# Kernel optimization log

Hardware: AMD Instinct MI355X
Metric: run time of the kernel (lower is better)

Reference implementation:

```python
import jax, jax.numpy as jnp
import numpy as np

N_NODES = 16384
N_EDGES = 131072
N_GRAPHS = 64
DIMS = [396, 4096, 2048, 1024, 1024, 2048, 256, 1]  # layer widths from __init__
BN_EPS = 1e-5


def setup_inputs() -> dict:
    key = jax.random.key(0)
    ks = jax.random.split(key, 32)
    inp = {
        "x": jax.random.normal(ks[0], (N_NODES, DIMS[0]), jnp.float32),
        "edge_index": jax.random.randint(ks[1], (2, N_EDGES), 0, N_NODES, dtype=jnp.int32),
        "batch": jnp.sort(jax.random.randint(ks[2], (N_NODES,), 0, N_GRAPHS, dtype=jnp.int32)),
    }
    for i in range(7):
        fi, fo = DIMS[i], DIMS[i + 1]
        inp[f"W{i+1}"] = jax.random.normal(ks[3 + i], (fi, fo), jnp.float32) * (1.0 / np.sqrt(fi)).astype(np.float32)
        inp[f"b{i+1}"] = jnp.zeros((fo,), jnp.float32)
    for i in range(6):
        inp[f"g{i+1}"] = jnp.ones((DIMS[i + 1],), jnp.float32)
        inp[f"be{i+1}"] = jnp.zeros((DIMS[i + 1],), jnp.float32)
    return inp


def _gcn_norm(edge_index, n):
    # PyG GCNConv default: add self-loops, sym-normalize D^-1/2 (A+I) D^-1/2
    loop = jnp.arange(n, dtype=edge_index.dtype)
    src = jnp.concatenate([edge_index[0], loop])
    dst = jnp.concatenate([edge_index[1], loop])
    deg = jax.ops.segment_sum(jnp.ones_like(src, jnp.float32), dst, num_segments=n)
    dinv = jax.lax.rsqrt(jnp.maximum(deg, 1.0))  # deg >= 1 due to self-loops
    norm = dinv[src] * dinv[dst]  # [E + N]
    return src, dst, norm


def _gcn_conv(x, W, b, src, dst, norm, n):
    h = x @ W                                   # dense linear transform
    msg = h[src] * norm[:, None]                # gather + edge scaling
    agg = jax.ops.segment_sum(msg, dst, num_segments=n)  # scatter-add
    return agg + b


def _bn(x, g, b):
    # BatchNorm1d in training mode: biased batch variance
    m = jnp.mean(x, axis=0)
    v = jnp.mean(jnp.square(x - m), axis=0)
    return (x - m) * jax.lax.rsqrt(v + BN_EPS) * g + b


def reference(x, edge_index, batch,
              W1, b1, W2, b2, W3, b3, W4, b4, W5, b5, W6, b6, W7, b7,
              g1, be1, g2, be2, g3, be3, g4, be4, g5, be5, g6, be6):
    n = x.shape[0]
    src, dst, norm = _gcn_norm(edge_index, n)
    Ws = [W1, W2, W3, W4, W5, W6]
    bs = [b1, b2, b3, b4, b5, b6]
    gs = [g1, g2, g3, g4, g5, g6]
    bes = [be1, be2, be3, be4, be5, be6]
    h = x
    for W, b, g, be in zip(Ws, bs, gs, bes):
        h = jax.nn.relu(_gcn_conv(h, W, b, src, dst, norm, n))
        h = _bn(h, g, be)
    h = _gcn_conv(h, W7, b7, src, dst, norm, n)   # [N, 1], no relu/bn
    out = jax.ops.segment_sum(h, batch, num_segments=N_GRAPHS)  # global_add_pool
    return out
```

## Files before the change

kernel.cpp:

```cpp
#include <hip/hip_runtime.h>


#define NN 16384
#define NE 131072
#define NG 64

typedef unsigned int u32;
typedef unsigned short u16;
typedef __attribute__((ext_vector_type(8))) _Float16 half8;
typedef __attribute__((ext_vector_type(4))) float f32x4;
typedef __attribute__((ext_vector_type(8))) u16 us8;
typedef __attribute__((ext_vector_type(4))) u16 us4;
typedef __attribute__((ext_vector_type(2))) u16 us2;

#define AS1(p) ((const __attribute__((address_space(1))) void*)(p))
#define AS3(p) ((__attribute__((address_space(3))) void*)(p))

__device__ __forceinline__ float b2f(u16 h) {
    _Float16 x = __builtin_bit_cast(_Float16, h);
    return (float)x;
}
__device__ __forceinline__ u16 f2b(float f) {
    _Float16 x = (_Float16)f;
    return __builtin_bit_cast(u16, x);
}

template <int VW> struct VecU;
template <> struct VecU<8> { typedef us8 T; };
template <> struct VecU<4> { typedef us4 T; };
template <> struct VecU<2> { typedef us2 T; };
template <> struct VecU<1> { typedef u16 T; };

template <int VW>
__device__ __forceinline__ void loadf(const u16* p, float* f) {
    typename VecU<VW>::T v = *(const typename VecU<VW>::T*)p;
    if constexpr (VW == 1) {
        f[0] = b2f((u16)v);
    } else {
        #pragma unroll
        for (int j = 0; j < VW; ++j) f[j] = b2f(v[j]);
    }
}
template <int VW>
__device__ __forceinline__ void storef(u16* p, const float* f) {
    typename VecU<VW>::T v;
    if constexpr (VW == 1) {
        v = f2b(f[0]);
    } else {
        #pragma unroll
        for (int j = 0; j < VW; ++j) v[j] = f2b(f[j]);
    }
    *(typename VecU<VW>::T*)p = v;
}

__global__ void k_degi(const int* __restrict__ dst, int* __restrict__ deg) {
    int e = blockIdx.x * 256 + threadIdx.x;
    if (e < NE) atomicAdd(&deg[dst[e]], 1);
}
__global__ void k_nrm(const int* __restrict__ src, const int* __restrict__ dst,
                      const float* __restrict__ dinv, float* __restrict__ nrm) {
    int e = blockIdx.x * 256 + threadIdx.x;
    if (e < NE) nrm[e] = dinv[src[e]] * dinv[dst[e]];
}
__global__ __launch_bounds__(1024) void k_scan(const int* __restrict__ deg, int* __restrict__ rowptr,
                                               float* __restrict__ dinv) {
    __shared__ int part[1024];
    int t = threadIdx.x;
    int base = t * 16;
    int s = 0;
    #pragma unroll
    for (int j = 0; j < 16; ++j) {
        int d = deg[base + j];
        dinv[base + j] = rsqrtf((float)(d + 1));
        s += d;
    }
    part[t] = s;
    __syncthreads();
    for (int off = 1; off < 1024; off <<= 1) {
        int v = 0;
        if (t >= off) v = part[t - off];
        __syncthreads();
        part[t] += v;
        __syncthreads();
    }
    int run = part[t] - s;
    for (int j = 0; j < 16; ++j) { rowptr[base + j] = run; run += deg[base + j]; }
    if (t == 1023) rowptr[NN] = run;
}
__global__ void k_place(const int* __restrict__ src, const int* __restrict__ dst,
                        const float* __restrict__ nrm, const int* __restrict__ rowptr,
                        int* __restrict__ cursor, int* __restrict__ csr_src,
                        float* __restrict__ csr_w) {
    int e = blockIdx.x * 256 + threadIdx.x;
    if (e >= NE) return;
    int d = dst[e];
    int p = rowptr[d] + atomicAdd(&cursor[d], 1);
    csr_src[p] = src[e];
    csr_w[p] = nrm[e];
}

__global__ void k_x2b(const float* __restrict__ x, u16* __restrict__ xp) {
    int idx = blockIdx.x * 256 + threadIdx.x;
    int i = idx >> 9, c = idx & 511;
    float v = (c < 396) ? x[(size_t)i * 396 + c] : 0.f;
    xp[idx] = f2b(v);
}
__global__ void k_wt(const float* __restrict__ W, u16* __restrict__ Wt,
                     int Ksrc, int Kpad, int N) {
    __shared__ float t[32][33];
    int k0 = blockIdx.x * 32, n0 = blockIdx.y * 32;
    int tx = threadIdx.x, ty = threadIdx.y;
    #pragma unroll
    for (int j = 0; j < 4; ++j) {
        int k = k0 + ty + j * 8;
        float v = 0.f;
        if (k < Ksrc) v = W[(size_t)k * N + n0 + tx];
        t[ty + j * 8][tx] = v;
    }
    __syncthreads();
    #pragma unroll
    for (int j = 0; j < 4; ++j) {
        int n = n0 + ty + j * 8;
        int k = k0 + tx;
        Wt[(size_t)n * Kpad + k] = f2b(t[tx][ty + j * 8]);
    }
}

template <int VW>
__global__ __launch_bounds__(256) void k_agg(const u16* __restrict__ in, u16* __restrict__ out,
                                             const int* __restrict__ rowptr,
                                             const int* __restrict__ csr_src,
                                             const float* __restrict__ csr_w,
                                             const float* __restrict__ dinv,
                                             const float* __restrict__ svec,
                                             const float* __restrict__ bias,
                                             const float* __restrict__ av,
                                             const float* __restrict__ bvv,
                                             float* __restrict__ svw,
                                             int F, int mode) {
    int i = blockIdx.x;
    int c0 = threadIdx.x * VW;
    float acc[VW];
    float d2 = dinv[i]; d2 *= d2;
    float wsum = d2;
    {
        float v[VW];
        loadf<VW>(in + (size_t)i * F + c0, v);
        #pragma unroll
        for (int j = 0; j < VW; ++j) acc[j] = d2 * v[j];
    }
    int r0 = rowptr[i], r1 = rowptr[i + 1];
    int e = r0;
    if (r1 - r0 >= 2) {
        float acc2[VW];
        #pragma unroll
        for (int j = 0; j < VW; ++j) acc2[j] = 0.f;
        for (; e + 1 < r1; e += 2) {
            int sa = csr_src[e], sb = csr_src[e + 1];
            float wa = csr_w[e], wb = csr_w[e + 1];
            wsum += wa + wb;
            float va[VW], vb[VW];
            loadf<VW>(in + (size_t)sa * F + c0, va);
            loadf<VW>(in + (size_t)sb * F + c0, vb);
            #pragma unroll
            for (int j = 0; j < VW; ++j) { acc[j] += wa * va[j]; acc2[j] += wb * vb[j]; }
        }
        #pragma unroll
        for (int j = 0; j < VW; ++j) acc[j] += acc2[j];
    }
    for (; e < r1; ++e) {
        int s = csr_src[e];
        float w = csr_w[e];
        wsum += w;
        float v[VW];
        loadf<VW>(in + (size_t)s * F + c0, v);
        #pragma unroll
        for (int j = 0; j < VW; ++j) acc[j] += w * v[j];
    }
    if (mode == 1) {
        #pragma unroll
        for (int j = 0; j < VW; ++j) acc[j] = fmaxf(acc[j] + bias[c0 + j], 0.f);
    } else if (mode == 2) {
        float si = svec[i];
        #pragma unroll
        for (int j = 0; j < VW; ++j) acc[j] = av[c0 + j] * acc[j] + si * bvv[c0 + j];
    }
    storef<VW>(out + (size_t)i * F + c0, acc);
    if (svw && threadIdx.x == 0) svw[i] = wsum;
}

#define SROWS 64
template <int VW>
__global__ __launch_bounds__(256) void k_stats(const u16* __restrict__ h, float* __restrict__ s1,
                                               float* __restrict__ s2, int F) {
    int c0 = threadIdx.x * VW;
    int r0 = blockIdx.y * SROWS;
    float s[VW], q[VW];
    #pragma unroll
    for (int j = 0; j < VW; ++j) { s[j] = 0.f; q[j] = 0.f; }
    for (int r = r0; r < r0 + SROWS; ++r) {
        float v[VW];
        loadf<VW>(h + (size_t)r * F + c0, v);
        #pragma unroll
        for (int j = 0; j < VW; ++j) { s[j] += v[j]; q[j] += v[j] * v[j]; }
    }
    #pragma unroll
    for (int j = 0; j < VW; ++j) {
        atomicAdd(&s1[c0 + j], s[j]);
        atomicAdd(&s2[c0 + j], q[j]);
    }
}
__global__ void k_bnab(const float* __restrict__ s1, const float* __restrict__ s2,
                       const float* __restrict__ g, const float* __restrict__ be,
                       float* __restrict__ a, float* __restrict__ b, int F) {
    int c = blockIdx.x * 256 + threadIdx.x;
    if (c >= F) return;
    float m = s1[c] * (1.f / NN);
    float v = s2[c] * (1.f / NN) - m * m;
    float aa = g[c] * rsqrtf(v + 1e-5f);
    a[c] = aa;
    b[c] = be[c] - m * aa;
}
__global__ __launch_bounds__(256) void k_bnapply(u16* __restrict__ h, const float* __restrict__ s1,
                                                 const float* __restrict__ s2,
                                                 const float* __restrict__ g,
                                                 const float* __restrict__ be, int F) {
    size_t idx = blockIdx.x * (size_t)256 + threadIdx.x;
    int Fv = F >> 3;
    int c = (int)(idx % Fv) * 8;
    u16* p = h + idx * 8;
    float v[8];
    loadf<8>(p, v);
    #pragma unroll
    for (int j = 0; j < 8; ++j) {
        float m = s1[c + j] * (1.f / NN);
        float var = s2[c + j] * (1.f / NN) - m * m;
        float a = g[c + j] * rsqrtf(var + 1e-5f);
        v[j] = a * (v[j] - m) + be[c + j];
    }
    storef<8>(p, v);
}

__device__ __forceinline__ void stage16k(const char* gbase, size_t rs, int ktile, int h,
                                         char* slot, int tid) {
    size_t colb = (size_t)ktile * 128 + h * 64;
    #pragma unroll
    for (int i = 0; i < 2; ++i) {
        int G = i * 512 + tid;
        int r = G >> 2;
        int c = ((G & 3) - (r >> 1)) & 3;
        __builtin_amdgcn_global_load_lds(AS1(gbase + (size_t)r * rs + colb + c * 16),
                                         AS3(slot + i * 8192 + ((tid >> 6) << 10)), 16, 0, 0);
    }
}

__global__ __launch_bounds__(512, 2) void k_gemm256(const u16* __restrict__ A,
                                                    const u16* __restrict__ Wt,
                                                    const float* __restrict__ bias,
                                                    u16* __restrict__ C,
                                                    float* __restrict__ s1,
                                                    float* __restrict__ s2,
                                                    int K, int N, int bx, int fuse) {
    extern __shared__ __align__(16) char smem[];
    int nwg = gridDim.x;
    int chunk = nwg >> 3;
    int swz = (blockIdx.x & 7) * chunk + (blockIdx.x >> 3);
    int tx = swz % bx, ty = swz / bx;
    int tid = threadIdx.x;
    int wid = tid >> 6, lane = tid & 63;
    int wr = wid >> 2, wc = wid & 3;
    int lo = lane & 15, hi = lane >> 4;
    int sw = (((hi + (lo >> 1)) & 3) << 4);
    size_t row0 = (size_t)ty * 256;
    size_t col0 = (size_t)tx * 256;
    int nkt = K >> 6;

    const char* gA = (const char*)(A + row0 * K);
    const char* gB = (const char*)(Wt + col0 * K);
    size_t rs = (size_t)K * 2;

    const char* aA = smem + wr * 8192 + lo * 64 + sw;
    const char* bA = smem + 65536 + wc * 4096 + lo * 64 + sw;
#define ASL(b, h) (smem + (((b) * 2 + (h)) << 14))
#define BSL(b, h) (smem + 65536 + (((b) * 2 + (h)) << 14))

    f32x4 acc[8][4];
    #pragma unroll
    for (int m = 0; m < 8; ++m)
        #pragma unroll
        for (int n = 0; n < 4; ++n) acc[m][n] = {0.f, 0.f, 0.f, 0.f};
    half8 af[4], bf[4];

    stage16k(gA, rs, 0, 0, ASL(0, 0), tid);
    stage16k(gB, rs, 0, 0, BSL(0, 0), tid);
    stage16k(gA, rs, 0, 1, ASL(0, 1), tid);
    stage16k(gB, rs, 0, 1, BSL(0, 1), tid);
    stage16k(gA, rs, 1, 0, ASL(1, 0), tid);
    stage16k(gB, rs, 1, 0, BSL(1, 0), tid);
    asm volatile("s_waitcnt vmcnt(4)" ::: "memory");
    __builtin_amdgcn_sched_barrier(0);
    __builtin_amdgcn_s_barrier();

#define DS_LOADS(KK, MH)                                                                   \
    {                                                                                      \
        _Pragma("unroll") for (int j = 0; j < 4; ++j)                                      \
            af[j] = *(const half8*)(aA + buf * 32768 + (KK) * 16384 + (MH) * 4096 + j * 1024); \
        if ((MH) == 0) {                                                                   \
            _Pragma("unroll") for (int j = 0; j < 4; ++j)                                  \
                bf[j] = *(const half8*)(bA + buf * 32768 + (KK) * 16384 + j * 1024);       \
        }                                                                                  \
    }
#define MFMA_PHASE(MH)                                                                     \
    {                                                                                      \
        __builtin_amdgcn_s_setprio(1);                                                     \
        _Pragma("unroll") for (int j = 0; j < 4; ++j)                                      \
            _Pragma("unroll") for (int n = 0; n < 4; ++n)                                  \
                acc[(MH) * 4 + j][n] = __builtin_amdgcn_mfma_f32_16x16x32_f16(             \
                    af[j], bf[n], acc[(MH) * 4 + j][n], 0, 0, 0);                          \
        __builtin_amdgcn_s_setprio(0);                                                     \
    }
#define END_BARRIER                                                                        \
    {                                                                                      \
        asm volatile("" ::: "memory");                                                     \
        __builtin_amdgcn_s_barrier();                                                      \
    }

    for (int kt = 0; kt < nkt; ++kt) {
        int buf = kt & 1;
        DS_LOADS(0, 0);
        if (kt + 1 < nkt) {
            stage16k(gA, rs, kt + 1, 1, ASL(buf ^ 1, 1), tid);
            stage16k(gB, rs, kt + 1, 1, BSL(buf ^ 1, 1), tid);
        }
        MFMA_PHASE(0);
        END_BARRIER;
        DS_LOADS(0, 1);
        MFMA_PHASE(1);
        END_BARRIER;
        DS_LOADS(1, 0);
        if (kt + 2 < nkt) stage16k(gA, rs, kt + 2, 0, ASL(buf, 0), tid);
        MFMA_PHASE(0);
        END_BARRIER;
        DS_LOADS(1, 1);
        if (kt + 2 < nkt) stage16k(gB, rs, kt + 2, 0, BSL(buf, 0), tid);
        MFMA_PHASE(1);
        asm volatile("s_waitcnt vmcnt(4)" ::: "memory");
        __builtin_amdgcn_sched_barrier(0);
        END_BARRIER;
    }

    float cs[4] = {0.f, 0.f, 0.f, 0.f}, cq[4] = {0.f, 0.f, 0.f, 0.f};
    #pragma unroll
    for (int fm = 0; fm < 8; ++fm) {
        #pragma unroll
        for (int n = 0; n < 4; ++n) {
            #pragma unroll
            for (int r = 0; r < 4; ++r) {
                size_t row = row0 + wr * 128 + fm * 16 + hi * 4 + r;
                size_t col = col0 + wc * 64 + n * 16 + lo;
                float v = acc[fm][n][r];
                if (fuse) v = fmaxf(v + bias[col], 0.f);
                C[row * N + col] = f2b(v);
                cs[n] += v;
                cq[n] += v * v;
            }
        }
    }
    if (s1) {
        asm volatile("s_waitcnt vmcnt(0)" ::: "memory");
        __syncthreads();
        float* sp = (float*)smem;
        sp[tid] = 0.f;
        __syncthreads();
        #pragma unroll
        for (int n = 0; n < 4; ++n) {
            int lc = wc * 64 + n * 16 + lo;
            atomicAdd(&sp[lc * 2], cs[n]);
            atomicAdd(&sp[lc * 2 + 1], cq[n]);
        }
        __syncthreads();
        if (tid < 256) {
            atomicAdd(&s1[col0 + tid], sp[tid * 2]);
            atomicAdd(&s2[col0 + tid], sp[tid * 2 + 1]);
        }
    }
#undef DS_LOADS
#undef MFMA_PHASE
#undef END_BARRIER
#undef ASL
#undef BSL
}

__global__ __launch_bounds__(256) void k_gemm(const u16* __restrict__ A, const u16* __restrict__ Wt,
                                              const float* __restrict__ bias, u16* __restrict__ C,
                                              int K, int N, int bx, int fuse) {
    __shared__ __align__(16) u16 As[128 * 32];
    __shared__ __align__(16) u16 Bs[128 * 32];
    int nwg = gridDim.x;
    int chunk = nwg >> 3;
    int swz = (blockIdx.x & 7) * chunk + (blockIdx.x >> 3);
    int tx = swz % bx, ty = swz / bx;
    int tid = threadIdx.x;
    int wid = tid >> 6, lane = tid & 63;
    int wr = wid >> 1, wc = wid & 1;
    int lo = lane & 15, hi = lane >> 4;
    size_t row0 = (size_t)ty * 128;
    size_t col0 = (size_t)tx * 128;

    f32x4 acc[4][4];
    #pragma unroll
    for (int m = 0; m < 4; ++m)
        #pragma unroll
        for (int n = 0; n < 4; ++n) acc[m][n] = {0.f, 0.f, 0.f, 0.f};

    const char* gA = (const char*)(A + row0 * K);
    const char* gB = (const char*)(Wt + col0 * K);
    size_t rs = (size_t)K * 2;
    int lin0 = tid * 16;
    int lin1 = lin0 + 4096;
    int rA0 = lin0 >> 6, cb0 = lin0 & 63;
    int rA1 = lin1 >> 6, cb1 = lin1 & 63;
    unsigned ldsOff = (unsigned)(wid << 10);

    for (int k0 = 0; k0 < K; k0 += 32) {
        __syncthreads();
        size_t kb = (size_t)k0 * 2;
        __builtin_amdgcn_global_load_lds(AS1(gA + (size_t)rA0 * rs + cb0 + kb),
                                         AS3((char*)As + ldsOff), 16, 0, 0);
        __builtin_amdgcn_global_load_lds(AS1(gA + (size_t)rA1 * rs + cb1 + kb),
                                         AS3((char*)As + 4096 + ldsOff), 16, 0, 0);
        __builtin_amdgcn_global_load_lds(AS1(gB + (size_t)rA0 * rs + cb0 + kb),
                                         AS3((char*)Bs + ldsOff), 16, 0, 0);
        __builtin_amdgcn_global_load_lds(AS1(gB + (size_t)rA1 * rs + cb1 + kb),
                                         AS3((char*)Bs + 4096 + ldsOff), 16, 0, 0);
        __syncthreads();
        half8 afr[4], bfr[4];
        #pragma unroll
        for (int m = 0; m < 4; ++m)
            afr[m] = *(const half8*)((const u16*)As + (wr * 64 + m * 16 + lo) * 32 + hi * 8);
        #pragma unroll
        for (int n = 0; n < 4; ++n)
            bfr[n] = *(const half8*)((const u16*)Bs + (wc * 64 + n * 16 + lo) * 32 + hi * 8);
        #pragma unroll
        for (int m = 0; m < 4; ++m)
            #pragma unroll
            for (int n = 0; n < 4; ++n)
                acc[m][n] = __builtin_amdgcn_mfma_f32_16x16x32_f16(afr[m], bfr[n], acc[m][n], 0, 0, 0);
    }
    #pragma unroll
    for (int m = 0; m < 4; ++m) {
        #pragma unroll
        for (int n = 0; n < 4; ++n) {
            #pragma unroll
            for (int r = 0; r < 4; ++r) {
                size_t row = row0 + wr * 64 + m * 16 + hi * 4 + r;
                size_t col = col0 + wc * 64 + n * 16 + lo;
                float v = acc[m][n][r];
                if (fuse) v = fmaxf(v + bias[col], 0.f);
                C[row * N + col] = f2b(v);
            }
        }
    }
}

__global__ __launch_bounds__(256) void k_gemv(const u16* __restrict__ A, const float* __restrict__ w,
                                              const float* __restrict__ a, const float* __restrict__ b,
                                              float* __restrict__ y) {
    int row = blockIdx.x * 4 + (threadIdx.x >> 6);
    int lane = threadIdx.x & 63;
    const u16* h = A + (size_t)row * 256;
    float s = 0.f;
    #pragma unroll
    for (int j = 0; j < 4; ++j) {
        int c = lane + j * 64;
        s += (a[c] * b2f(h[c]) + b[c]) * w[c];
    }
    #pragma unroll
    for (int off = 32; off; off >>= 1) s += __shfl_down(s, off);
    if (lane == 0) y[row] = s;
}
__global__ void k_final(const float* __restrict__ y, const int* __restrict__ rowptr,
                        const int* __restrict__ csr_src, const float* __restrict__ csr_w,
                        const float* __restrict__ dinv, const int* __restrict__ batch,
                        const float* __restrict__ b7, float* __restrict__ out) {
    int i = blockIdx.x * 256 + threadIdx.x;
    if (i >= NN) return;
    float v = dinv[i] * dinv[i] * y[i];
    int r1 = rowptr[i + 1];
    for (int e = rowptr[i]; e < r1; ++e) v += csr_w[e] * y[csr_src[e]];
    atomicAdd(&out[batch[i]], v + b7[0]);
}
__global__ void k_sentinel(float* out, float v) {
    if (threadIdx.x == 0 && blockIdx.x == 0) out[0] = v;
}

static inline char* alignp(char* p) { return (char*)(((uintptr_t)p + 255) & ~(uintptr_t)255); }

extern "C" void kernel_launch(void* const* d_in, const int* in_sizes, int n_in,
                              void* d_out, int out_size, void* d_ws, size_t ws_size,
                              hipStream_t stream) {
    const float* x = (const float*)d_in[0];
    const int* ei = (const int*)d_in[1];
    const int* src = ei;
    const int* dst = ei + NE;
    const int* batch = (const int*)d_in[2];
    const float* W[7]; const float* bv[7];
    for (int i = 0; i < 7; ++i) { W[i] = (const float*)d_in[3 + 2 * i]; bv[i] = (const float*)d_in[4 + 2 * i]; }
    const float* g[6]; const float* be[6];
    for (int i = 0; i < 6; ++i) { g[i] = (const float*)d_in[17 + 2 * i]; be[i] = (const float*)d_in[18 + 2 * i]; }
    float* out = (float*)d_out;

    char* p = (char*)d_ws;
    u16* Abuf = (u16*)p; p += (size_t)NN * 4096 * 2;
    u16* Bbuf = (u16*)p; p += (size_t)NN * 2048 * 2;
    u16* xpad = (u16*)p; p += (size_t)NN * 512 * 2;
    u16* W1t = (u16*)p; p += (size_t)4096 * 512 * 2;
    u16* W2t = (u16*)p; p += (size_t)2048 * 4096 * 2;
    u16* W3t = (u16*)p; p += (size_t)1024 * 2048 * 2;
    u16* W4t = (u16*)p; p += (size_t)1024 * 1024 * 2;
    u16* W5t = (u16*)p; p += (size_t)2048 * 1024 * 2;
    u16* W6t = (u16*)p; p += (size_t)256 * 2048 * 2;
    p = alignp(p);
    int* degi = (int*)p; p += NN * 4;
    int* cursor = (int*)p; p += NN * 4;
    int* rowptr = (int*)p; p += (NN + 1) * 4; p = alignp(p);
    int* csr_src = (int*)p; p += NE * 4;
    float* csr_w = (float*)p; p += NE * 4;
    float* dinv = (float*)p; p += NN * 4;
    float* nrm = (float*)p; p += NE * 4;
    float* svec = (float*)p; p += NN * 4;
    float* s1 = (float*)p; p += 4096 * 4;
    float* s2 = (float*)p; p += 4096 * 4;
    float* bna = (float*)p; p += 4096 * 4;
    float* bnb = (float*)p; p += 4096 * 4;
    float* y = (float*)p; p += NN * 4;
    size_t need = (size_t)(p - (char*)d_ws);
    if (need > ws_size) {
        hipMemsetAsync(d_out, 0, NG * sizeof(float), stream);
        k_sentinel<<<1, 64, 0, stream>>>(out, (float)(ws_size >> 20));
        return;
    }

    (void)hipFuncSetAttribute((const void*)k_gemm256,
                              hipFuncAttributeMaxDynamicSharedMemorySize, 131072);

    hipMemsetAsync(degi, 0, 2 * NN * sizeof(int), stream);
    k_degi<<<NE / 256, 256, 0, stream>>>(dst, degi);
    k_scan<<<1, 1024, 0, stream>>>(degi, rowptr, dinv);
    k_nrm<<<NE / 256, 256, 0, stream>>>(src, dst, dinv, nrm);
    k_place<<<NE / 256, 256, 0, stream>>>(src, dst, nrm, rowptr, cursor, csr_src, csr_w);

    k_x2b<<<(NN * 512) / 256, 256, 0, stream>>>(x, xpad);
    dim3 wtb(32, 8);
    k_wt<<<dim3(16, 128), wtb, 0, stream>>>(W[0], W1t, 396, 512, 4096);
    k_wt<<<dim3(128, 64), wtb, 0, stream>>>(W[1], W2t, 4096, 4096, 2048);
    k_wt<<<dim3(64, 32), wtb, 0, stream>>>(W[2], W3t, 2048, 2048, 1024);
    k_wt<<<dim3(32, 32), wtb, 0, stream>>>(W[3], W4t, 1024, 1024, 1024);
    k_wt<<<dim3(32, 64), wtb, 0, stream>>>(W[4], W5t, 1024, 1024, 2048);
    k_wt<<<dim3(64, 8), wtb, 0, stream>>>(W[5], W6t, 2048, 2048, 256);

    auto gemm256 = [&](const u16* A, const u16* Wt, const float* bias, u16* Cp,
                       float* st1, float* st2, int K, int N, int fuse) {
        int bx = N / 256;
        k_gemm256<<<bx * (NN / 256), 512, 131072, stream>>>(A, Wt, bias, Cp, st1, st2, K, N, bx, fuse);
    };
    auto agg = [&](const u16* in, u16* o, const float* bias, const float* av,
                   const float* bvv, float* svw, int F, int mode) {
        if (F >= 512) k_agg<8><<<NN, F / 8, 0, stream>>>(in, o, rowptr, csr_src, csr_w, dinv, svec, bias, av, bvv, svw, F, mode);
        else k_agg<4><<<NN, F / 4, 0, stream>>>(in, o, rowptr, csr_src, csr_w, dinv, svec, bias, av, bvv, svw, F, mode);
    };
    auto stats = [&](const u16* h, int F) {
        hipMemsetAsync(s1, 0, 2 * 4096 * sizeof(float), stream);
        if (F >= 512) k_stats<8><<<dim3(1, NN / SROWS), F / 8, 0, stream>>>(h, s1, s2, F);
        else k_stats<4><<<dim3(1, NN / SROWS), F / 4, 0, stream>>>(h, s1, s2, F);
    };
    auto bnapply = [&](u16* h, int F, int li) {
        k_bnapply<<<(int)(((size_t)NN * F / 8) / 256), 256, 0, stream>>>(h, s1, s2, g[li], be[li], F);
    };

    agg(xpad, Bbuf, nullptr, nullptr, nullptr, svec, 512, 0);
    hipMemsetAsync(s1, 0, 2 * 4096 * sizeof(float), stream);
    gemm256(Bbuf, W1t, bv[0], Abuf, s1, s2, 512, 4096, 1);
    bnapply(Abuf, 4096, 0);

    gemm256(Abuf, W2t, nullptr, Bbuf, nullptr, nullptr, 4096, 2048, 0);
    agg(Bbuf, Abuf, bv[1], nullptr, nullptr, nullptr, 2048, 1);
    stats(Abuf, 2048);
    bnapply(Abuf, 2048, 1);

    gemm256(Abuf, W3t, nullptr, Bbuf, nullptr, nullptr, 2048, 1024, 0);
    agg(Bbuf, Abuf, bv[2], nullptr, nullptr, nullptr, 1024, 1);
    stats(Abuf, 1024);
    bnapply(Abuf, 1024, 2);

    gemm256(Abuf, W4t, nullptr, Bbuf, nullptr, nullptr, 1024, 1024, 0);
    agg(Bbuf, Abuf, bv[3], nullptr, nullptr, nullptr, 1024, 1);
    stats(Abuf, 1024);
    k_bnab<<<1024 / 256, 256, 0, stream>>>(s1, s2, g[3], be[3], bna, bnb, 1024);

    agg(Abuf, Bbuf, nullptr, bna, bnb, nullptr, 1024, 2);
    hipMemsetAsync(s1, 0, 2 * 4096 * sizeof(float), stream);
    gemm256(Bbuf, W5t, bv[4], Abuf, s1, s2, 1024, 2048, 1);
    bnapply(Abuf, 2048, 4);

    k_gemm<<<(256 / 128) * (NN / 128), 256, 0, stream>>>(Abuf, W6t, nullptr, Bbuf, 2048, 256, 256 / 128, 0);
    agg(Bbuf, Abuf, bv[5], nullptr, nullptr, nullptr, 256, 1);
    stats(Abuf, 256);
    k_bnab<<<1, 256, 0, stream>>>(s1, s2, g[5], be[5], bna, bnb, 256);

    k_gemv<<<NN / 4, 256, 0, stream>>>(Abuf, W[6], bna, bnb, y);
    hipMemsetAsync(d_out, 0, NG * sizeof(float), stream);
    k_final<<<NN / 256, 256, 0, stream>>>(y, rowptr, csr_src, csr_w, dinv, batch, bv[6], out);
}
```

Before: 1.498 ms.

## Merge GEMM k-loop phases, inline BN coefficients, vectorize x conversion

The 256-tile GEMM main loop now loads both M halves of the A fragments at once and issues all 32 MFMAs per K-substep. This halves the number of LDS-load/barrier phases per K tile and stages the next A and B tiles together, at the cost of more fragment registers. The separate k_bnab kernels are removed and BN scale/shift is recomputed inline in the aggregation and GEMV kernels. The input conversion kernel now writes 8 halves per thread, and the stats row chunk is doubled.

```diff
diff --git a/kernel.cpp b/kernel.cpp
--- a/kernel.cpp
+++ b/kernel.cpp
@@ -51,6 +51,14 @@
         for (int j = 0; j < VW; ++j) v[j] = f2b(f[j]);
     }
     *(typename VecU<VW>::T*)p = v;
+}
+
+__device__ __forceinline__ void bn_ab(float s1c, float s2c, float gc, float bec,
+                                      float& a, float& b) {
+    float m = s1c * (1.f / NN);
+    float var = s2c * (1.f / NN) - m * m;
+    a = gc * rsqrtf(var + 1e-5f);
+    b = bec - m * a;
 }
 
 __global__ void k_degi(const int* __restrict__ dst, int* __restrict__ deg) {
@@ -101,9 +109,15 @@
 
 __global__ void k_x2b(const float* __restrict__ x, u16* __restrict__ xp) {
     int idx = blockIdx.x * 256 + threadIdx.x;
-    int i = idx >> 9, c = idx & 511;
-    float v = (c < 396) ? x[(size_t)i * 396 + c] : 0.f;
-    xp[idx] = f2b(v);
+    int i = idx >> 6, cg = idx & 63;
+    int c0 = cg * 8;
+    float v[8];
+    #pragma unroll
+    for (int j = 0; j < 8; ++j) {
+        int c = c0 + j;
+        v[j] = (c < 396) ? x[(size_t)i * 396 + c] : 0.f;
+    }
+    storef<8>(xp + (size_t)i * 512 + c0, v);
 }
 __global__ void k_wt(const float* __restrict__ W, u16* __restrict__ Wt,
                      int Ksrc, int Kpad, int N) {
@@ -134,8 +148,10 @@
                                              const float* __restrict__ dinv,
                                              const float* __restrict__ svec,
                                              const float* __restrict__ bias,
-                                             const float* __restrict__ av,
-                                             const float* __restrict__ bvv,
+                                             const float* __restrict__ s1,
+                                             const float* __restrict__ s2,
+                                             const float* __restrict__ g,
+                                             const float* __restrict__ be,
                                              float* __restrict__ svw,
                                              int F, int mode) {
     int i = blockIdx.x;
@@ -183,13 +199,17 @@
     } else if (mode == 2) {
         float si = svec[i];
         #pragma unroll
-        for (int j = 0; j < VW; ++j) acc[j] = av[c0 + j] * acc[j] + si * bvv[c0 + j];
+        for (int j = 0; j < VW; ++j) {
+            float a, b;
+            bn_ab(s1[c0 + j], s2[c0 + j], g[c0 + j], be[c0 + j], a, b);
+            acc[j] = a * acc[j] + si * b;
+        }
     }
     storef<VW>(out + (size_t)i * F + c0, acc);
     if (svw && threadIdx.x == 0) svw[i] = wsum;
 }
 
-#define SROWS 64
+#define SROWS 128
 template <int VW>
 __global__ __launch_bounds__(256) void k_stats(const u16* __restrict__ h, float* __restrict__ s1,
                                                float* __restrict__ s2, int F) {
@@ -209,17 +229,6 @@
         atomicAdd(&s1[c0 + j], s[j]);
         atomicAdd(&s2[c0 + j], q[j]);
     }
-}
-__global__ void k_bnab(const float* __restrict__ s1, const float* __restrict__ s2,
-                       const float* __restrict__ g, const float* __restrict__ be,
-                       float* __restrict__ a, float* __restrict__ b, int F) {
-    int c = blockIdx.x * 256 + threadIdx.x;
-    if (c >= F) return;
-    float m = s1[c] * (1.f / NN);
-    float v = s2[c] * (1.f / NN) - m * m;
-    float aa = g[c] * rsqrtf(v + 1e-5f);
-    a[c] = aa;
-    b[c] = be[c] - m * aa;
 }
 __global__ __launch_bounds__(256) void k_bnapply(u16* __restrict__ h, const float* __restrict__ s1,
                                                  const float* __restrict__ s2,
@@ -233,10 +242,9 @@
     loadf<8>(p, v);
     #pragma unroll
     for (int j = 0; j < 8; ++j) {
-        float m = s1[c + j] * (1.f / NN);
-        float var = s2[c + j] * (1.f / NN) - m * m;
-        float a = g[c + j] * rsqrtf(var + 1e-5f);
-        v[j] = a * (v[j] - m) + be[c + j];
+        float a, b;
+        bn_ab(s1[c + j], s2[c + j], g[c + j], be[c + j], a, b);
+        v[j] = a * v[j] + b;
     }
     storef<8>(p, v);
 }
@@ -289,7 +297,7 @@
     for (int m = 0; m < 8; ++m)
         #pragma unroll
         for (int n = 0; n < 4; ++n) acc[m][n] = {0.f, 0.f, 0.f, 0.f};
-    half8 af[4], bf[4];
+    half8 af0[4], af1[4], bf[4];
 
     stage16k(gA, rs, 0, 0, ASL(0, 0), tid);
     stage16k(gB, rs, 0, 0, BSL(0, 0), tid);
@@ -301,22 +309,26 @@
     __builtin_amdgcn_sched_barrier(0);
     __builtin_amdgcn_s_barrier();
 
-#define DS_LOADS(KK, MH)                                                                   \
+#define DS_LOADS2(KK)                                                                      \
     {                                                                                      \
         _Pragma("unroll") for (int j = 0; j < 4; ++j)                                      \
-            af[j] = *(const half8*)(aA + buf * 32768 + (KK) * 16384 + (MH) * 4096 + j * 1024); \
-        if ((MH) == 0) {                                                                   \
-            _Pragma("unroll") for (int j = 0; j < 4; ++j)                                  \
-                bf[j] = *(const half8*)(bA + buf * 32768 + (KK) * 16384 + j * 1024);       \
-        }                                                                                  \
-    }
-#define MFMA_PHASE(MH)                                                                     \
+            af0[j] = *(const half8*)(aA + buf * 32768 + (KK) * 16384 + j * 1024);          \
+        _Pragma("unroll") for (int j = 0; j < 4; ++j)                                      \
+            af1[j] = *(const half8*)(aA + buf * 32768 + (KK) * 16384 + 4096 + j * 1024);   \
+        _Pragma("unroll") for (int j = 0; j < 4; ++j)                                      \
+            bf[j] = *(const half8*)(bA + buf * 32768 + (KK) * 16384 + j * 1024);           \
+    }
+#define MFMA_BOTH                                                                          \
     {                                                                                      \
         __builtin_amdgcn_s_setprio(1);                                                     \
         _Pragma("unroll") for (int j = 0; j < 4; ++j)                                      \
             _Pragma("unroll") for (int n = 0; n < 4; ++n)                                  \
-                acc[(MH) * 4 + j][n] = __builtin_amdgcn_mfma_f32_16x16x32_f16(             \
-                    af[j], bf[n], acc[(MH) * 4 + j][n], 0, 0, 0);                          \
+                acc[j][n] = __builtin_amdgcn_mfma_f32_16x16x32_f16(                        \
+                    af0[j], bf[n], acc[j][n], 0, 0, 0);                                    \
+        _Pragma("unroll") for (int j = 0; j < 4; ++j)                                      \
+            _Pragma("unroll") for (int n = 0; n < 4; ++n)                                  \
+                acc[4 + j][n] = __builtin_amdgcn_mfma_f32_16x16x32_f16(                    \
+                    af1[j], bf[n], acc[4 + j][n], 0, 0, 0);                                \
         __builtin_amdgcn_s_setprio(0);                                                     \
     }
 #define END_BARRIER                                                                        \
@@ -327,23 +339,19 @@
 
     for (int kt = 0; kt < nkt; ++kt) {
         int buf = kt & 1;
-        DS_LOADS(0, 0);
+        DS_LOADS2(0);
         if (kt + 1 < nkt) {
             stage16k(gA, rs, kt + 1, 1, ASL(buf ^ 1, 1), tid);
             stage16k(gB, rs, kt + 1, 1, BSL(buf ^ 1, 1), tid);
         }
-        MFMA_PHASE(0);
+        MFMA_BOTH;
         END_BARRIER;
-        DS_LOADS(0, 1);
-        MFMA_PHASE(1);
-        END_BARRIER;
-        DS_LOADS(1, 0);
-        if (kt + 2 < nkt) stage16k(gA, rs, kt + 2, 0, ASL(buf, 0), tid);
-        MFMA_PHASE(0);
-        END_BARRIER;
-        DS_LOADS(1, 1);
-        if (kt + 2 < nkt) stage16k(gB, rs, kt + 2, 0, BSL(buf, 0), tid);
-        MFMA_PHASE(1);
+        DS_LOADS2(1);
+        if (kt + 2 < nkt) {
+            stage16k(gA, rs, kt + 2, 0, ASL(buf, 0), tid);
+            stage16k(gB, rs, kt + 2, 0, BSL(buf, 0), tid);
+        }
+        MFMA_BOTH;
         asm volatile("s_waitcnt vmcnt(4)" ::: "memory");
         __builtin_amdgcn_sched_barrier(0);
         END_BARRIER;
@@ -384,8 +392,8 @@
             atomicAdd(&s2[col0 + tid], sp[tid * 2 + 1]);
         }
     }
-#undef DS_LOADS
-#undef MFMA_PHASE
+#undef DS_LOADS2
+#undef MFMA_BOTH
 #undef END_BARRIER
 #undef ASL
 #undef BSL
@@ -464,7 +472,8 @@
 }
 
 __global__ __launch_bounds__(256) void k_gemv(const u16* __restrict__ A, const float* __restrict__ w,
-                                              const float* __restrict__ a, const float* __restrict__ b,
+                                              const float* __restrict__ s1, const float* __restrict__ s2,
+                                              const float* __restrict__ g, const float* __restrict__ be,
                                               float* __restrict__ y) {
     int row = blockIdx.x * 4 + (threadIdx.x >> 6);
     int lane = threadIdx.x & 63;
@@ -473,7 +482,9 @@
     #pragma unroll
     for (int j = 0; j < 4; ++j) {
         int c = lane + j * 64;
-        s += (a[c] * b2f(h[c]) + b[c]) * w[c];
+        float a, b;
+        bn_ab(s1[c], s2[c], g[c], be[c], a, b);
+        s += (a * b2f(h[c]) + b) * w[c];
     }
     #pragma unroll
     for (int off = 32; off; off >>= 1) s += __shfl_down(s, off);
@@ -531,8 +542,6 @@
     float* svec = (float*)p; p += NN * 4;
     float* s1 = (float*)p; p += 4096 * 4;
     float* s2 = (float*)p; p += 4096 * 4;
-    float* bna = (float*)p; p += 4096 * 4;
-    float* bnb = (float*)p; p += 4096 * 4;
     float* y = (float*)p; p += NN * 4;
     size_t need = (size_t)(p - (char*)d_ws);
     if (need > ws_size) {
@@ -550,7 +559,7 @@
     k_nrm<<<NE / 256, 256, 0, stream>>>(src, dst, dinv, nrm);
     k_place<<<NE / 256, 256, 0, stream>>>(src, dst, nrm, rowptr, cursor, csr_src, csr_w);
 
-    k_x2b<<<(NN * 512) / 256, 256, 0, stream>>>(x, xpad);
+    k_x2b<<<(NN * 64) / 256, 256, 0, stream>>>(x, xpad);
     dim3 wtb(32, 8);
     k_wt<<<dim3(16, 128), wtb, 0, stream>>>(W[0], W1t, 396, 512, 4096);
     k_wt<<<dim3(128, 64), wtb, 0, stream>>>(W[1], W2t, 4096, 4096, 2048);
@@ -564,10 +573,12 @@
         int bx = N / 256;
         k_gemm256<<<bx * (NN / 256), 512, 131072, stream>>>(A, Wt, bias, Cp, st1, st2, K, N, bx, fuse);
     };
-    auto agg = [&](const u16* in, u16* o, const float* bias, const float* av,
-                   const float* bvv, float* svw, int F, int mode) {
-        if (F >= 512) k_agg<8><<<NN, F / 8, 0, stream>>>(in, o, rowptr, csr_src, csr_w, dinv, svec, bias, av, bvv, svw, F, mode);
-        else k_agg<4><<<NN, F / 4, 0, stream>>>(in, o, rowptr, csr_src, csr_w, dinv, svec, bias, av, bvv, svw, F, mode);
+    auto agg = [&](const u16* in, u16* o, const float* bias, int li, float* svw,
+                   int F, int mode) {
+        const float* gp = (mode == 2) ? g[li] : nullptr;
+        const float* bep = (mode == 2) ? be[li] : nullptr;
+        if (F >= 512) k_agg<8><<<NN, F / 8, 0, stream>>>(in, o, rowptr, csr_src, csr_w, dinv, svec, bias, s1, s2, gp, bep, svw, F, mode);
+        else k_agg<4><<<NN, F / 4, 0, stream>>>(in, o, rowptr, csr_src, csr_w, dinv, svec, bias, s1, s2, gp, bep, svw, F, mode);
     };
     auto stats = [&](const u16* h, int F) {
         hipMemsetAsync(s1, 0, 2 * 4096 * sizeof(float), stream);
@@ -578,37 +589,35 @@
         k_bnapply<<<(int)(((size_t)NN * F / 8) / 256), 256, 0, stream>>>(h, s1, s2, g[li], be[li], F);
     };
 
-    agg(xpad, Bbuf, nullptr, nullptr, nullptr, svec, 512, 0);
+    agg(xpad, Bbuf, nullptr, 0, svec, 512, 0);
     hipMemsetAsync(s1, 0, 2 * 4096 * sizeof(float), stream);
     gemm256(Bbuf, W1t, bv[0], Abuf, s1, s2, 512, 4096, 1);
     bnapply(Abuf, 4096, 0);
 
     gemm256(Abuf, W2t, nullptr, Bbuf, nullptr, nullptr, 4096, 2048, 0);
-    agg(Bbuf, Abuf, bv[1], nullptr, nullptr, nullptr, 2048, 1);
+    agg(Bbuf, Abuf, bv[1], 1, nullptr, 2048, 1);
     stats(Abuf, 2048);
     bnapply(Abuf, 2048, 1);
 
     gemm256(Abuf, W3t, nullptr, Bbuf, nullptr, nullptr, 2048, 1024, 0);
-    agg(Bbuf, Abuf, bv[2], nullptr, nullptr, nullptr, 1024, 1);
+    agg(Bbuf, Abuf, bv[2], 2, nullptr, 1024, 1);
     stats(Abuf, 1024);
     bnapply(Abuf, 1024, 2);
 
     gemm256(Abuf, W4t, nullptr, Bbuf, nullptr, nullptr, 1024, 1024, 0);
-    agg(Bbuf, Abuf, bv[3], nullptr, nullptr, nullptr, 1024, 1);
+    agg(Bbuf, Abuf, bv[3], 3, nullptr, 1024, 1);
     stats(Abuf, 1024);
-    k_bnab<<<1024 / 256, 256, 0, stream>>>(s1, s2, g[3], be[3], bna, bnb, 1024);
-
-    agg(Abuf, Bbuf, nullptr, bna, bnb, nullptr, 1024, 2);
+
+    agg(Abuf, Bbuf, nullptr, 3, nullptr, 1024, 2);
     hipMemsetAsync(s1, 0, 2 * 4096 * sizeof(float), stream);
     gemm256(Bbuf, W5t, bv[4], Abuf, s1, s2, 1024, 2048, 1);
     bnapply(Abuf, 2048, 4);
 
     k_gemm<<<(256 / 128) * (NN / 128), 256, 0, stream>>>(Abuf, W6t, nullptr, Bbuf, 2048, 256, 256 / 128, 0);
-    agg(Bbuf, Abuf, bv[5], nullptr, nullptr, nullptr, 256, 1);
+    agg(Bbuf, Abuf, bv[5], 5, nullptr, 256, 1);
     stats(Abuf, 256);
-    k_bnab<<<1, 256, 0, stream>>>(s1, s2, g[5], be[5], bna, bnb, 256);
-
-    k_gemv<<<NN / 4, 256, 0, stream>>>(Abuf, W[6], bna, bnb, y);
+
+    k_gemv<<<NN / 4, 256, 0, stream>>>(Abuf, W[6], s1, s2, g[5], be[5], y);
     hipMemsetAsync(d_out, 0, NG * sizeof(float), stream);
     k_final<<<NN / 256, 256, 0, stream>>>(y, rowptr, csr_src, csr_w, dinv, batch, bv[6], out);
 }
```

Result: faster. 1.406 ms, median of 2 (-6.1%).
